# Optimization experiments

Hardware: AMD Instinct MI355X
Metric: run time of the kernel (lower is better)

Reference implementation:

```python
import jax, jax.numpy as jnp
import numpy as np
import math

B, S, E, H = 2, 2048, 1024, 16
D = E // H  # head dim = 64


def setup_inputs() -> dict:
    key = jax.random.key(0)
    ks = jax.random.split(key, 7)
    scale = 1.0 / math.sqrt(E)
    return {
        "query": jax.random.normal(ks[0], (B, S, E), dtype=jnp.float32),
        "key": jax.random.normal(ks[1], (B, S, E), dtype=jnp.float32),
        "value": jax.random.normal(ks[2], (B, S, E), dtype=jnp.float32),
        # packed in-projection: (3E, E) weights, (3E,) bias, q/k/v order
        "in_proj_weight": jax.random.normal(ks[3], (3 * E, E), dtype=jnp.float32) * scale,
        "in_proj_bias": jnp.zeros((3 * E,), dtype=jnp.float32),
        "out_proj_weight": jax.random.normal(ks[4], (E, E), dtype=jnp.float32) * scale,
        "out_proj_bias": jnp.zeros((E,), dtype=jnp.float32),
    }


def reference(query, key, value, in_proj_weight, in_proj_bias, out_proj_weight, out_proj_bias):
    # packed in-projection (q, k, v order), F.linear convention: x @ W^T + b
    w_q, w_k, w_v = jnp.split(in_proj_weight, 3, axis=0)
    b_q, b_k, b_v = jnp.split(in_proj_bias, 3, axis=0)
    q = query @ w_q.T + b_q   # [B, S, E]
    k = key @ w_k.T + b_k
    v = value @ w_v.T + b_v

    # split heads: [B, S, E] -> [B, H, S, D]
    def heads(x):
        return x.reshape(B, S, H, D).transpose(0, 2, 1, 3)

    q, k, v = heads(q), heads(k), heads(v)
    q = q / jnp.asarray(math.sqrt(D), dtype=q.dtype)

    # naive softmax attention (materializes [B, H, S, S] as original bmm+softmax+bmm)
    scores = jnp.einsum("bhqd,bhkd->bhqk", q, k)
    attn = jax.nn.softmax(scores, axis=-1)
    out = jnp.einsum("bhqk,bhkd->bhqd", attn, v)  # [B, H, S, D]

    out = out.transpose(0, 2, 1, 3).reshape(B, S, E)
    return out @ out_proj_weight.T + out_proj_bias
```

## Files before the change

kernel.cpp:

```cpp
#include <hip/hip_runtime.h>
#include <stdint.h>

#define LOG2E 1.44269504088896340736f

typedef __bf16 bf16x8 __attribute__((ext_vector_type(8)));
typedef float f32x4 __attribute__((ext_vector_type(4)));
typedef float f32x16 __attribute__((ext_vector_type(16)));

static constexpr int Bb = 2, Ss = 2048, Ee = 1024, Hh = 16, Dd = 64;
static constexpr int BSE = Bb * Ss * Ee;

static constexpr size_t OFF_QB    = 0;
static constexpr size_t OFF_KB    = 4194304;
static constexpr size_t OFF_VB    = 8388608;
static constexpr size_t OFF_WQKV  = 12582912;
static constexpr size_t OFF_WOUT  = 15728640;
static constexpr size_t OFF_QH    = 16777216;
static constexpr size_t OFF_KH    = 20971520;
static constexpr size_t OFF_VH    = 25165824;
static constexpr size_t OFF_OB    = 29360128;

__device__ __forceinline__ uint16_t f32_bf16(float f) {
    uint32_t u = __builtin_bit_cast(uint32_t, f);
    u += 0x7fffu + ((u >> 16) & 1u);
    return (uint16_t)(u >> 16);
}

__device__ __forceinline__ uint32_t cvt_pk_bf16(float a, float b) {
    uint32_t r;
    asm("v_cvt_pk_bf16_f32 %0, %1, %2" : "=v"(r) : "v"(a), "v"(b));
    return r;
}

__device__ __forceinline__ void perm32swap(uint32_t& x, uint32_t& y) {
    asm("v_permlane32_swap_b32 %0, %1" : "+v"(x), "+v"(y));
}

__global__ __launch_bounds__(256) void cvt_kernel(
    const float* __restrict__ q, const float* __restrict__ k, const float* __restrict__ v,
    const float* __restrict__ w1, const float* __restrict__ w2, uint16_t* __restrict__ ws)
{
    const float* srcs[5] = {q, k, v, w1, w2};
    const int ns4[5] = {BSE/4, BSE/4, BSE/4, (3*Ee*Ee)/4, (Ee*Ee)/4};
    uint16_t* dsts[5] = {ws+OFF_QB, ws+OFF_KB, ws+OFF_VB, ws+OFF_WQKV, ws+OFF_WOUT};
    int z = blockIdx.z;
    int i = blockIdx.x * blockDim.x + threadIdx.x;
    if (i < ns4[z]) {
        float4 f = ((const float4*)srcs[z])[i];
        ushort4 o;
        o.x = f32_bf16(f.x); o.y = f32_bf16(f.y);
        o.z = f32_bf16(f.z); o.w = f32_bf16(f.w);
        ((ushort4*)dsts[z])[i] = o;
    }
}

template<int MODE, int BM>
__global__ __launch_bounds__(256) void gemm_nt(
    const uint16_t* __restrict__ Aq, const uint16_t* __restrict__ Ak,
    const uint16_t* __restrict__ Av, const uint16_t* __restrict__ Bw,
    const float* __restrict__ bias, uint16_t* __restrict__ OutB,
    float* __restrict__ OutF)
{
    constexpr int K = Ee, N = Ee;
    constexpr int M4 = BM / 32;
    const int tid = threadIdx.x;
    const int l = tid & 63, w = tid >> 6;
    const int wr = w >> 1, wc = w & 1;
    const int z = (MODE == 0) ? blockIdx.z : 0;
    int tm, tn;
    if (MODE == 0) { tm = 4 * blockIdx.x + (blockIdx.y >> 3); tn = blockIdx.y & 7; }
    else           { tm = (blockIdx.y >> 3) * 8 + blockIdx.x; tn = blockIdx.y & 7; }

    const uint16_t* A = (MODE == 0) ? (z == 0 ? Aq : (z == 1 ? Ak : Av)) : Aq;
    const uint16_t* Bp = Bw + (size_t)z * Ee * Ee;
    const float* bp = bias + (size_t)z * Ee;
    const size_t zoff = (size_t)(z == 2 ? 3 : z) * BSE;

    __shared__ alignas(16) uint16_t As[BM * 32];
    __shared__ alignas(16) uint16_t Bs[128 * 32];

    f32x4 acc[M4][4] = {};
    const int arow = tm * BM;
    const int bcol = tn * 128;

    for (int kt = 0; kt < K / 32; ++kt) {
        __syncthreads();
        #pragma unroll
        for (int it = 0; it < BM / 64; ++it) {
            int c = tid + it * 256;
            int row = c >> 2, qq = c & 3;
            const uint16_t* ga = A + (size_t)(arow + row) * K + kt * 32 + qq * 8;
            __builtin_amdgcn_global_load_lds(
                (const __attribute__((address_space(1))) void*)ga,
                (__attribute__((address_space(3))) void*)(As + c * 8), 16, 0, 0);
        }
        #pragma unroll
        for (int it = 0; it < 2; ++it) {
            int c = tid + it * 256;
            int row = c >> 2, qq = c & 3;
            const uint16_t* gb = Bp + (size_t)(bcol + row) * K + kt * 32 + qq * 8;
            __builtin_amdgcn_global_load_lds(
                (const __attribute__((address_space(1))) void*)gb,
                (__attribute__((address_space(3))) void*)(Bs + c * 8), 16, 0, 0);
        }
        __syncthreads();
        bf16x8 aF[M4], bF[4];
        #pragma unroll
        for (int m = 0; m < M4; ++m)
            aF[m] = *(const bf16x8*)(As + ((wr * (BM / 2) + m * 16 + (l & 15)) * 32 + (l >> 4) * 8));
        #pragma unroll
        for (int n = 0; n < 4; ++n)
            bF[n] = *(const bf16x8*)(Bs + ((wc * 64 + n * 16 + (l & 15)) * 32 + (l >> 4) * 8));
        #pragma unroll
        for (int m = 0; m < M4; ++m)
            #pragma unroll
            for (int n = 0; n < 4; ++n)
                acc[m][n] = __builtin_amdgcn_mfma_f32_16x16x32_bf16(aF[m], bF[n], acc[m][n], 0, 0, 0);
    }

    #pragma unroll
    for (int n = 0; n < 4; ++n) {
        int col = bcol + wc * 64 + n * 16 + (l & 15);
        float bn = bp[col];
        #pragma unroll
        for (int m = 0; m < M4; ++m) {
            int row0 = arow + wr * (BM / 2) + m * 16 + (l >> 4) * 4;
            #pragma unroll
            for (int j = 0; j < 4; ++j) {
                int row = row0 + j;
                float v = acc[m][n][j] + bn;
                if (MODE == 0) {
                    if (z == 0) v *= 0.125f * LOG2E;
                    int b = row >> 11, s = row & 2047, hh = col >> 6, d = col & 63;
                    OutB[zoff + (size_t)(((b * Hh) + hh) * Ss + s) * Dd + d] = f32_bf16(v);
                } else {
                    OutF[(size_t)row * N + col] = v;
                }
            }
        }
    }
}

__global__ __launch_bounds__(256) void vtr_kernel(
    const uint16_t* __restrict__ src, uint16_t* __restrict__ dst)
{
    __shared__ uint32_t T32[64][33];
    const int tid = threadIdx.x;
    const int bh = blockIdx.y;
    const int s0 = blockIdx.x * 64;
    const uint16_t* S = src + ((size_t)bh * Ss + s0) * Dd;
    {
        int rp = tid >> 3, d8 = tid & 7;
        uint4 a = *(const uint4*)(S + (size_t)(2 * rp) * Dd + d8 * 8);
        uint4 b = *(const uint4*)(S + (size_t)(2 * rp + 1) * Dd + d8 * 8);
        const uint16_t* ea = (const uint16_t*)&a;
        const uint16_t* eb = (const uint16_t*)&b;
        #pragma unroll
        for (int e = 0; e < 8; ++e)
            T32[d8 * 8 + e][rp] = (uint32_t)ea[e] | ((uint32_t)eb[e] << 16);
    }
    __syncthreads();
    uint16_t* Dp = dst + (size_t)bh * Dd * Ss + s0;
    {
        int d = tid >> 3, rpc = (tid & 7) * 4;
        #pragma unroll
        for (int half = 0; half < 2; ++half) {
            int dd = d + 32 * half;
            union { uint32_t u[4]; uint4 v; } pk;
            #pragma unroll
            for (int j = 0; j < 4; ++j) pk.u[j] = T32[dd][rpc + j];
            *(uint4*)(Dp + (size_t)dd * Ss + rpc * 2) = pk.v;
        }
    }
}

__global__ __launch_bounds__(256, 2) void attn_kernel(
    const uint16_t* __restrict__ Qh, const uint16_t* __restrict__ Kh,
    const uint16_t* __restrict__ Vtg, uint16_t* __restrict__ Ob)
{
    const int tid = threadIdx.x;
    const int l = tid & 63, w = tid >> 6;
    const int q = l & 31, hi = l >> 5;

    const int orig = blockIdx.x;
    const int L = (orig & 7) * 64 + (orig >> 3);
    const int qb = L & 15, bh = L >> 4;

    const int q0 = qb * 128;
    const size_t baseK = (size_t)bh * Ss * Dd;
    const size_t baseV = (size_t)bh * Dd * Ss;

    __shared__ alignas(16) uint16_t Ks[3][64 * 64];
    __shared__ alignas(16) uint16_t Vt[3][64 * 64];

    bf16x8 qf[4];
    {
        const uint16_t* qp = Qh + baseK + (size_t)(q0 + w * 32 + q) * Dd + hi * 8;
        #pragma unroll
        for (int m = 0; m < 4; ++m) qf[m] = *(const bf16x8*)(qp + 16 * m);
    }

    auto stage = [&](int kt, int buf) {
        const int key0 = kt * 64;
        #pragma unroll
        for (int it = 0; it < 2; ++it) {
            int c = tid + 256 * it, row = c >> 3, cc = c & 7;
            const uint16_t* gk = Kh + baseK + (size_t)(key0 + row) * Dd + ((cc ^ (row & 7)) * 8);
            __builtin_amdgcn_global_load_lds(
                (const __attribute__((address_space(1))) void*)gk,
                (__attribute__((address_space(3))) void*)(&Ks[buf][c * 8]), 16, 0, 0);
        }
        #pragma unroll
        for (int it = 0; it < 2; ++it) {
            int c = tid + 256 * it, d = c >> 3, j = c & 7;
            const uint16_t* gv = Vtg + baseV + (size_t)d * Ss + key0 + 8 * (j ^ (d & 7) ^ (d >> 3));
            __builtin_amdgcn_global_load_lds(
                (const __attribute__((address_space(1))) void*)gv,
                (__attribute__((address_space(3))) void*)(&Vt[buf][c * 8]), 16, 0, 0);
        }
    };

    stage(0, 0);
    stage(1, 1);

    f32x16 o0 = {}, o1 = {};
    float lsum = 0.f;

    auto build_pb = [&](const f32x16& sv, bf16x8* pbout) {
        uint32_t W[4][2];
        #pragma unroll
        for (int a = 0; a < 4; ++a) {
            float p0 = __builtin_amdgcn_exp2f(sv[4 * a + 0]);
            float p1 = __builtin_amdgcn_exp2f(sv[4 * a + 1]);
            float p2 = __builtin_amdgcn_exp2f(sv[4 * a + 2]);
            float p3 = __builtin_amdgcn_exp2f(sv[4 * a + 3]);
            lsum += (p0 + p1) + (p2 + p3);
            W[a][0] = cvt_pk_bf16(p0, p1);
            W[a][1] = cvt_pk_bf16(p2, p3);
        }
        #pragma unroll
        for (int kl = 0; kl < 2; ++kl) {
            uint32_t x0 = W[2 * kl][0], x1 = W[2 * kl][1];
            uint32_t y0 = W[2 * kl + 1][0], y1 = W[2 * kl + 1][1];
            perm32swap(x0, y0);
            perm32swap(x1, y1);
            union { uint32_t u[4]; bf16x8 v; } pu;
            pu.u[0] = x0; pu.u[1] = x1; pu.u[2] = y0; pu.u[3] = y1;
            pbout[kl] = pu.v;
        }
    };

    auto body = [&](int kt, int b, int bs, bool doIssue, bool last) {
        if (last) asm volatile("s_waitcnt vmcnt(0)" ::: "memory");
        else      asm volatile("s_waitcnt vmcnt(4)" ::: "memory");
        __builtin_amdgcn_s_barrier();
        __builtin_amdgcn_sched_barrier(0);

        if (doIssue) stage(kt + 2, bs);

        f32x16 s0 = {}, s1 = {};
        __builtin_amdgcn_s_setprio(1);
        #pragma unroll
        for (int m = 0; m < 4; ++m) {
            int sw = ((2 * m + hi) ^ (q & 7)) << 3;
            bf16x8 k0 = *(const bf16x8*)&Ks[b][q * 64 + sw];
            bf16x8 k1 = *(const bf16x8*)&Ks[b][(32 + q) * 64 + sw];
            s0 = __builtin_amdgcn_mfma_f32_32x32x16_bf16(k0, qf[m], s0, 0, 0, 0);
            s1 = __builtin_amdgcn_mfma_f32_32x32x16_bf16(k1, qf[m], s1, 0, 0, 0);
        }
        __builtin_amdgcn_s_setprio(0);

        bf16x8 pb[4];
        build_pb(s0, pb + 0);
        build_pb(s1, pb + 2);

        __builtin_amdgcn_s_setprio(1);
        #pragma unroll
        for (int ka = 0; ka < 4; ++ka) {
            #pragma unroll
            for (int dt = 0; dt < 2; ++dt) {
                int d = 32 * dt + q;
                int swz = (2 * ka + hi) ^ (d & 7) ^ (d >> 3);
                bf16x8 vf = *(const bf16x8*)&Vt[b][d * 64 + swz * 8];
                if (dt == 0)
                    o0 = __builtin_amdgcn_mfma_f32_32x32x16_bf16(vf, pb[ka], o0, 0, 0, 0);
                else
                    o1 = __builtin_amdgcn_mfma_f32_32x32x16_bf16(vf, pb[ka], o1, 0, 0, 0);
            }
        }
        __builtin_amdgcn_s_setprio(0);
    };

    for (int u = 0; u < 30; u += 3) {
        body(u + 0, 0, 2, true, false);
        body(u + 1, 1, 0, true, false);
        body(u + 2, 2, 1, true, false);
    }
    body(30, 0, 0, false, false);
    body(31, 1, 0, false, true);

    float lr = lsum + __shfl_xor(lsum, 32);
    const float inv = 1.0f / lr;
    __syncthreads();
    uint16_t* Os = &Ks[0][0];
    const int ql = w * 32 + q;
    #pragma unroll
    for (int dt = 0; dt < 2; ++dt) {
        const f32x16& oo = dt ? o1 : o0;
        #pragma unroll
        for (int rr = 0; rr < 16; ++rr) {
            int d = 32 * dt + (rr & 3) + 8 * (rr >> 2) + 4 * hi;
            Os[ql * 64 + (((d >> 3) ^ (ql & 7)) << 3) + (d & 7)] = f32_bf16(oo[rr] * inv);
        }
    }
    __syncthreads();
    const int bq = bh >> 4, hh = bh & 15;
    #pragma unroll
    for (int it = 0; it < 4; ++it) {
        int qr = it * 32 + (tid >> 3);
        int c = tid & 7;
        bf16x8 vv = *(const bf16x8*)&Os[qr * 64 + ((c ^ (qr & 7)) << 3)];
        *(bf16x8*)(Ob + (size_t)(bq * Ss + q0 + qr) * Ee + hh * Dd + c * 8) = vv;
    }
}

extern "C" void kernel_launch(void* const* d_in, const int* in_sizes, int n_in,
                              void* d_out, int out_size, void* d_ws, size_t ws_size,
                              hipStream_t stream) {
    (void)in_sizes; (void)n_in; (void)out_size; (void)ws_size;
    const float* query = (const float*)d_in[0];
    const float* key   = (const float*)d_in[1];
    const float* value = (const float*)d_in[2];
    const float* w_in  = (const float*)d_in[3];
    const float* b_in  = (const float*)d_in[4];
    const float* w_out = (const float*)d_in[5];
    const float* b_out = (const float*)d_in[6];
    uint16_t* ws = (uint16_t*)d_ws;

    uint16_t* qb    = ws + OFF_QB;
    uint16_t* kb    = ws + OFF_KB;
    uint16_t* vb    = ws + OFF_VB;
    uint16_t* wqkvb = ws + OFF_WQKV;
    uint16_t* woutb = ws + OFF_WOUT;
    uint16_t* Qh    = ws + OFF_QH;
    uint16_t* Kh    = ws + OFF_KH;
    uint16_t* Vtg   = ws + OFF_VH;
    uint16_t* Vsd   = ws + OFF_OB;
    uint16_t* Ob    = ws + OFF_OB;

    cvt_kernel<<<dim3(4096, 1, 5), 256, 0, stream>>>(query, key, value, w_in, w_out, ws);
    gemm_nt<0, 128><<<dim3(8, 32, 3), 256, 0, stream>>>(qb, kb, vb, wqkvb, b_in, Qh, nullptr);
    vtr_kernel<<<dim3(32, 32), 256, 0, stream>>>(Vsd, Vtg);
    attn_kernel<<<dim3(512), 256, 0, stream>>>(Qh, Kh, Vtg, Ob);
    gemm_nt<1, 64><<<dim3(8, 64), 256, 0, stream>>>(Ob, nullptr, nullptr, woutb, b_out, nullptr, (float*)d_out);
}
```

Baseline: 123.8 us.

## Software-pipeline QK of next tile with softmax and PV of current tile

Restructures the attention inner loop so that the QK^T MFMAs for tile kt+1 are issued while the exp/pack and PV MFMAs for tile kt run. The aim is to hide the exponential and conversion latency behind matrix work. As a trade-off, the wait before each iteration becomes vmcnt(0) instead of vmcnt(4), which waits on the most recent prefetch and may expose load latency. The extra live score accumulators also raise register pressure.

```diff
diff --git a/kernel.cpp b/kernel.cpp
--- a/kernel.cpp
+++ b/kernel.cpp
@@ -220,11 +220,21 @@
         }
     };
 
-    stage(0, 0);
-    stage(1, 1);
-
     f32x16 o0 = {}, o1 = {};
     float lsum = 0.f;
+
+    auto qk = [&](int b, f32x16& s0, f32x16& s1) {
+        __builtin_amdgcn_s_setprio(1);
+        #pragma unroll
+        for (int m = 0; m < 4; ++m) {
+            int sw = ((2 * m + hi) ^ (q & 7)) << 3;
+            bf16x8 k0 = *(const bf16x8*)&Ks[b][q * 64 + sw];
+            bf16x8 k1 = *(const bf16x8*)&Ks[b][(32 + q) * 64 + sw];
+            s0 = __builtin_amdgcn_mfma_f32_32x32x16_bf16(k0, qf[m], s0, 0, 0, 0);
+            s1 = __builtin_amdgcn_mfma_f32_32x32x16_bf16(k1, qf[m], s1, 0, 0, 0);
+        }
+        __builtin_amdgcn_s_setprio(0);
+    };
 
     auto build_pb = [&](const f32x16& sv, bf16x8* pbout) {
         uint32_t W[4][2];
@@ -250,30 +260,7 @@
         }
     };
 
-    auto body = [&](int kt, int b, int bs, bool doIssue, bool last) {
-        if (last) asm volatile("s_waitcnt vmcnt(0)" ::: "memory");
-        else      asm volatile("s_waitcnt vmcnt(4)" ::: "memory");
-        __builtin_amdgcn_s_barrier();
-        __builtin_amdgcn_sched_barrier(0);
-
-        if (doIssue) stage(kt + 2, bs);
-
-        f32x16 s0 = {}, s1 = {};
-        __builtin_amdgcn_s_setprio(1);
-        #pragma unroll
-        for (int m = 0; m < 4; ++m) {
-            int sw = ((2 * m + hi) ^ (q & 7)) << 3;
-            bf16x8 k0 = *(const bf16x8*)&Ks[b][q * 64 + sw];
-            bf16x8 k1 = *(const bf16x8*)&Ks[b][(32 + q) * 64 + sw];
-            s0 = __builtin_amdgcn_mfma_f32_32x32x16_bf16(k0, qf[m], s0, 0, 0, 0);
-            s1 = __builtin_amdgcn_mfma_f32_32x32x16_bf16(k1, qf[m], s1, 0, 0, 0);
-        }
-        __builtin_amdgcn_s_setprio(0);
-
-        bf16x8 pb[4];
-        build_pb(s0, pb + 0);
-        build_pb(s1, pb + 2);
-
+    auto pv = [&](int b, const bf16x8* pb) {
         __builtin_amdgcn_s_setprio(1);
         #pragma unroll
         for (int ka = 0; ka < 4; ++ka) {
@@ -291,13 +278,38 @@
         __builtin_amdgcn_s_setprio(0);
     };
 
+    stage(0, 0);
+    stage(1, 1);
+    f32x16 sc0 = {}, sc1 = {};
+    asm volatile("s_waitcnt vmcnt(4)" ::: "memory");
+    __builtin_amdgcn_s_barrier();
+    __builtin_amdgcn_sched_barrier(0);
+    qk(0, sc0, sc1);
+
+    auto body = [&](int kt, int b, int bn, int bs, bool doStage, bool doNext) {
+        asm volatile("s_waitcnt vmcnt(0)" ::: "memory");
+        __builtin_amdgcn_s_barrier();
+        __builtin_amdgcn_sched_barrier(0);
+        if (doStage) stage(kt + 2, bs);
+
+        bf16x8 pb[4];
+        build_pb(sc0, pb + 0);
+        build_pb(sc1, pb + 2);
+
+        f32x16 sn0 = {}, sn1 = {};
+        if (doNext) qk(bn, sn0, sn1);
+
+        pv(b, pb);
+        sc0 = sn0; sc1 = sn1;
+    };
+
     for (int u = 0; u < 30; u += 3) {
-        body(u + 0, 0, 2, true, false);
-        body(u + 1, 1, 0, true, false);
-        body(u + 2, 2, 1, true, false);
-    }
-    body(30, 0, 0, false, false);
-    body(31, 1, 0, false, true);
+        body(u + 0, 0, 1, 2, true, true);
+        body(u + 1, 1, 2, 0, true, true);
+        body(u + 2, 2, 0, 1, true, true);
+    }
+    body(30, 0, 1, 0, false, true);
+    body(31, 1, 0, 0, false, false);
 
     float lr = lsum + __shfl_xor(lsum, 32);
     const float inv = 1.0f / lr;
```

New measurement: 120.7 us. 2.4% less time.

## Double key tile to 128 with double buffering and interleaved QK/PV halves

Applied to the files above, without the earlier changes.

The attention inner loop now processes 128 keys per iteration instead of 64, using two LDS buffers of 128-key K and V^T tiles instead of three 64-key buffers. This halves the number of barrier and wait points and lets the second half's QK MFMAs be issued before the first half's softmax and PV work, to improve overlap. In exchange, LDS use per block grows and prefetch depth drops to one tile, with a full vmcnt(0) wait each iteration. This could expose more global-load latency.

```diff
diff --git a/kernel.cpp b/kernel.cpp
--- a/kernel.cpp
+++ b/kernel.cpp
@@ -190,8 +190,8 @@
     const size_t baseK = (size_t)bh * Ss * Dd;
     const size_t baseV = (size_t)bh * Dd * Ss;
 
-    __shared__ alignas(16) uint16_t Ks[3][64 * 64];
-    __shared__ alignas(16) uint16_t Vt[3][64 * 64];
+    __shared__ alignas(16) uint16_t Ks[2][128 * 64];
+    __shared__ alignas(16) uint16_t Vt[2][64 * 128];
 
     bf16x8 qf[4];
     {
@@ -201,9 +201,9 @@
     }
 
     auto stage = [&](int kt, int buf) {
-        const int key0 = kt * 64;
-        #pragma unroll
-        for (int it = 0; it < 2; ++it) {
+        const int key0 = kt * 128;
+        #pragma unroll
+        for (int it = 0; it < 4; ++it) {
             int c = tid + 256 * it, row = c >> 3, cc = c & 7;
             const uint16_t* gk = Kh + baseK + (size_t)(key0 + row) * Dd + ((cc ^ (row & 7)) * 8);
             __builtin_amdgcn_global_load_lds(
@@ -211,8 +211,8 @@
                 (__attribute__((address_space(3))) void*)(&Ks[buf][c * 8]), 16, 0, 0);
         }
         #pragma unroll
-        for (int it = 0; it < 2; ++it) {
-            int c = tid + 256 * it, d = c >> 3, j = c & 7;
+        for (int it = 0; it < 4; ++it) {
+            int c = tid + 256 * it, d = c >> 4, j = c & 15;
             const uint16_t* gv = Vtg + baseV + (size_t)d * Ss + key0 + 8 * (j ^ (d & 7) ^ (d >> 3));
             __builtin_amdgcn_global_load_lds(
                 (const __attribute__((address_space(1))) void*)gv,
@@ -220,13 +220,23 @@
         }
     };
 
-    stage(0, 0);
-    stage(1, 1);
-
     f32x16 o0 = {}, o1 = {};
-    float lsum = 0.f;
-
-    auto build_pb = [&](const f32x16& sv, bf16x8* pbout) {
+    float lsumA = 0.f, lsumB = 0.f;
+
+    auto qk_half = [&](int b, int rowoff, f32x16& s0, f32x16& s1) {
+        __builtin_amdgcn_s_setprio(1);
+        #pragma unroll
+        for (int m = 0; m < 4; ++m) {
+            int sw = ((2 * m + hi) ^ (q & 7)) << 3;
+            bf16x8 k0 = *(const bf16x8*)&Ks[b][(rowoff + q) * 64 + sw];
+            bf16x8 k1 = *(const bf16x8*)&Ks[b][(rowoff + 32 + q) * 64 + sw];
+            s0 = __builtin_amdgcn_mfma_f32_32x32x16_bf16(k0, qf[m], s0, 0, 0, 0);
+            s1 = __builtin_amdgcn_mfma_f32_32x32x16_bf16(k1, qf[m], s1, 0, 0, 0);
+        }
+        __builtin_amdgcn_s_setprio(0);
+    };
+
+    auto build_pb = [&](const f32x16& sv, bf16x8* pbout, float& lsum) {
         uint32_t W[4][2];
         #pragma unroll
         for (int a = 0; a < 4; ++a) {
@@ -250,55 +260,52 @@
         }
     };
 
-    auto body = [&](int kt, int b, int bs, bool doIssue, bool last) {
-        if (last) asm volatile("s_waitcnt vmcnt(0)" ::: "memory");
-        else      asm volatile("s_waitcnt vmcnt(4)" ::: "memory");
-        __builtin_amdgcn_s_barrier();
-        __builtin_amdgcn_sched_barrier(0);
-
-        if (doIssue) stage(kt + 2, bs);
-
-        f32x16 s0 = {}, s1 = {};
+    auto pv_half = [&](int b, const bf16x8* pb, int ka0) {
         __builtin_amdgcn_s_setprio(1);
         #pragma unroll
-        for (int m = 0; m < 4; ++m) {
-            int sw = ((2 * m + hi) ^ (q & 7)) << 3;
-            bf16x8 k0 = *(const bf16x8*)&Ks[b][q * 64 + sw];
-            bf16x8 k1 = *(const bf16x8*)&Ks[b][(32 + q) * 64 + sw];
-            s0 = __builtin_amdgcn_mfma_f32_32x32x16_bf16(k0, qf[m], s0, 0, 0, 0);
-            s1 = __builtin_amdgcn_mfma_f32_32x32x16_bf16(k1, qf[m], s1, 0, 0, 0);
-        }
-        __builtin_amdgcn_s_setprio(0);
-
-        bf16x8 pb[4];
-        build_pb(s0, pb + 0);
-        build_pb(s1, pb + 2);
-
-        __builtin_amdgcn_s_setprio(1);
-        #pragma unroll
-        for (int ka = 0; ka < 4; ++ka) {
+        for (int kk = 0; kk < 4; ++kk) {
+            int jl = 2 * (ka0 + kk) + hi;
             #pragma unroll
             for (int dt = 0; dt < 2; ++dt) {
                 int d = 32 * dt + q;
-                int swz = (2 * ka + hi) ^ (d & 7) ^ (d >> 3);
-                bf16x8 vf = *(const bf16x8*)&Vt[b][d * 64 + swz * 8];
+                int phys = jl ^ (d & 7) ^ (d >> 3);
+                bf16x8 vf = *(const bf16x8*)&Vt[b][d * 128 + phys * 8];
                 if (dt == 0)
-                    o0 = __builtin_amdgcn_mfma_f32_32x32x16_bf16(vf, pb[ka], o0, 0, 0, 0);
+                    o0 = __builtin_amdgcn_mfma_f32_32x32x16_bf16(vf, pb[kk], o0, 0, 0, 0);
                 else
-                    o1 = __builtin_amdgcn_mfma_f32_32x32x16_bf16(vf, pb[ka], o1, 0, 0, 0);
+                    o1 = __builtin_amdgcn_mfma_f32_32x32x16_bf16(vf, pb[kk], o1, 0, 0, 0);
             }
         }
         __builtin_amdgcn_s_setprio(0);
     };
 
-    for (int u = 0; u < 30; u += 3) {
-        body(u + 0, 0, 2, true, false);
-        body(u + 1, 1, 0, true, false);
-        body(u + 2, 2, 1, true, false);
-    }
-    body(30, 0, 0, false, false);
-    body(31, 1, 0, false, true);
-
+    stage(0, 0);
+
+    for (int kt = 0; kt < 16; ++kt) {
+        const int b = kt & 1;
+        asm volatile("s_waitcnt vmcnt(0)" ::: "memory");
+        __builtin_amdgcn_s_barrier();
+        __builtin_amdgcn_sched_barrier(0);
+        if (kt < 15) stage(kt + 1, b ^ 1);
+
+        f32x16 s0 = {}, s1 = {}, s2 = {}, s3 = {};
+        qk_half(b, 0, s0, s1);
+        qk_half(b, 64, s2, s3);
+
+        bf16x8 pbA[4];
+        build_pb(s0, pbA + 0, lsumA);
+        build_pb(s1, pbA + 2, lsumA);
+
+        pv_half(b, pbA, 0);
+
+        bf16x8 pbB[4];
+        build_pb(s2, pbB + 0, lsumB);
+        build_pb(s3, pbB + 2, lsumB);
+
+        pv_half(b, pbB, 4);
+    }
+
+    float lsum = lsumA + lsumB;
     float lr = lsum + __shfl_xor(lsum, 32);
     const float inv = 1.0f / lr;
     __syncthreads();
```

After: 122.7 us. Within noise of the previous version (-0.8%).
